# Optimization experiments

Hardware: AMD Instinct MI355X
Metric: run time of the kernel (lower is better)

Reference implementation:

```python
import jax, jax.numpy as jnp
import numpy as np
from jax import lax

B, T_IN, T_OUT = 64, 200, 400
D_ENC, D_ARNN, D_DRNN = 512, 1024, 1024
PRENET, ATT_DIM, NFILT, KSIZE, NMEL = 256, 128, 32, 31, 80


def setup_inputs() -> dict:
    key = jax.random.key(0)
    ks = jax.random.split(key, 20)
    sc = lambda k, shape: (jax.random.normal(k, shape, jnp.float32) * 0.02)
    lengths = jnp.maximum(jax.random.randint(ks[0], (B,), 0, T_IN), T_IN // 2)
    return {
        'encoder_outputs': jax.random.normal(ks[1], (B, T_IN, D_ENC), jnp.float32),
        'decoder_inputs': jax.random.normal(ks[2], (T_OUT, B, NMEL), jnp.float32),
        'encoder_outputs_lengths': lengths,
        'W_p1': sc(ks[3], (PRENET, NMEL)),
        'W_p2': sc(ks[4], (PRENET, PRENET)),
        'W_ih_a': sc(ks[5], (4 * D_ARNN, PRENET + D_ENC)),
        'W_hh_a': sc(ks[6], (4 * D_ARNN, D_ARNN)),
        'b_a': jnp.zeros((4 * D_ARNN,), jnp.float32),
        'Wq': sc(ks[7], (ATT_DIM, D_ARNN)),
        'Wmem': sc(ks[8], (ATT_DIM, D_ENC)),
        'v': sc(ks[9], (ATT_DIM,)),
        'Wconv': sc(ks[10], (NFILT, 2, KSIZE)),
        'Wloc': sc(ks[11], (ATT_DIM, NFILT)),
        'W_ih_d': sc(ks[12], (4 * D_DRNN, D_ARNN + D_ENC)),
        'W_hh_d': sc(ks[13], (4 * D_DRNN, D_DRNN)),
        'b_d': jnp.zeros((4 * D_DRNN,), jnp.float32),
        'Wp': sc(ks[14], (NMEL, D_DRNN + D_ENC)),
        'bp': jnp.zeros((NMEL,), jnp.float32),
    }


def _lstm_cell(x, h, c, Wih, Whh, b):
    g = x @ Wih.T + h @ Whh.T + b
    i, f, gg, o = jnp.split(g, 4, axis=-1)
    c_new = jax.nn.sigmoid(f) * c + jax.nn.sigmoid(i) * jnp.tanh(gg)
    h_new = jax.nn.sigmoid(o) * jnp.tanh(c_new)
    return h_new, c_new


def reference(encoder_outputs, decoder_inputs, encoder_outputs_lengths,
              W_p1, W_p2, W_ih_a, W_hh_a, b_a, Wq, Wmem, v, Wconv, Wloc,
              W_ih_d, W_hh_d, b_d, Wp, bp):
    Bsz, T_in, _ = encoder_outputs.shape
    T_steps = decoder_inputs.shape[0]
    NEG = jnp.float32(-1e8)
    pad = (KSIZE - 1) // 2

    # go frame + prenet (prenet_dropout = 0.0 => pure relu MLP)
    go = jnp.zeros((1, Bsz, NMEL), decoder_inputs.dtype)
    di = jnp.concatenate([go, decoder_inputs], axis=0)          # [T+1, B, 80]
    pre = jax.nn.relu(jax.nn.relu(di @ W_p1.T) @ W_p2.T)        # [T+1, B, 256]
    xs = pre[:T_steps]                                          # step i uses pre[i]

    processed_memory = encoder_outputs @ Wmem.T                 # [B, T_in, att]
    mask = jnp.arange(T_in)[None, :] >= encoder_outputs_lengths[:, None]

    def step(carry, x_t):
        ah, ac, dh, dc, aw, aw_cum, actx = carry
        cell_in = jnp.concatenate([x_t, actx], axis=-1)
        ah, ac = _lstm_cell(cell_in, ah, ac, W_ih_a, W_hh_a, b_a)
        # location-sensitive attention
        awc = jnp.stack([aw, aw_cum], axis=1)                   # [B, 2, T_in]
        loc = lax.conv_general_dilated(awc, Wconv, (1,), [(pad, pad)],
                                       dimension_numbers=('NCH', 'OIH', 'NCH'))
        loc = jnp.swapaxes(loc, 1, 2) @ Wloc.T                  # [B, T_in, att]
        pq = (ah @ Wq.T)[:, None, :]                            # [B, 1, att]
        energies = jnp.tanh(pq + loc + processed_memory) @ v    # [B, T_in]
        energies = jnp.where(mask, NEG, energies)
        aw = jax.nn.softmax(energies, axis=1)
        actx = jnp.einsum('bt,bte->be', aw, encoder_outputs)
        aw_cum = aw_cum + aw
        dec_in = jnp.concatenate([ah, actx], axis=-1)
        dh, dc = _lstm_cell(dec_in, dh, dc, W_ih_d, W_hh_d, b_d)
        out = jnp.concatenate([dh, actx], axis=-1) @ Wp.T + bp  # [B, 80]
        return (ah, ac, dh, dc, aw, aw_cum, actx), (out, aw)

    z = lambda d: jnp.zeros((Bsz, d), encoder_outputs.dtype)
    carry0 = (z(D_ARNN), z(D_ARNN), z(D_DRNN), z(D_DRNN), z(T_in), z(T_in), z(D_ENC))
    _, (outs, aligns) = lax.scan(step, carry0, xs)
    return jnp.swapaxes(outs, 0, 1), jnp.swapaxes(aligns, 0, 1)  # [B,T,80], [B,T,T_in]
```

## Files before the change

### kernel.cpp

```cpp
#include <hip/hip_runtime.h>
#include <cstddef>
#include <cstdint>

#define T_INN 200
#define T_OUTT 400
#define BB 64
#define DENC 512
#define NMEL 80

typedef unsigned short u16;
typedef __bf16 bf16x8 __attribute__((ext_vector_type(8)));
typedef float f32x4 __attribute__((ext_vector_type(4)));

__device__ __forceinline__ float sigf(float x) {
  return __builtin_amdgcn_rcpf(1.0f + __expf(-x));
}
__device__ __forceinline__ float ftanh(float x) {
  float e2 = __expf(2.0f * x);
  return 1.0f - 2.0f * __builtin_amdgcn_rcpf(e2 + 1.0f);
}

__device__ __forceinline__ u16 f2bf(float f) {
  unsigned u = __float_as_uint(f);
  unsigned r = u + 0x7fffu + ((u >> 16) & 1u);
  return (u16)(r >> 16);
}

__device__ __forceinline__ bf16x8 ldbf8(const u16* p) { return *(const bf16x8*)p; }

__global__ __launch_bounds__(256) void gemm_pre_kernel(
    const float* __restrict__ A, int lda, const float* __restrict__ W, int ldw,
    float* __restrict__ C, u16* __restrict__ Cbf, int ldc, int K, int relu)
{
  __shared__ float As[16][66];
  __shared__ float Ws[16][66];
  const int tid = threadIdx.x;
  const int tn = tid & 15, tm = tid >> 4;
  const int n0 = blockIdx.x * 64;
  const int m0 = blockIdx.y * 64;
  float acc[4][4] = {{0.f}};
  for (int kt = 0; kt < K; kt += 16) {
#pragma unroll
    for (int i = 0; i < 4; i++) {
      int e = tid + 256 * i;
      int m = e >> 4, kk = e & 15;
      As[kk][m] = A[(size_t)(m0 + m) * lda + kt + kk];
    }
#pragma unroll
    for (int i = 0; i < 4; i++) {
      int e = tid + 256 * i;
      int n = e >> 4, kk = e & 15;
      Ws[kk][n] = W[(size_t)(n0 + n) * ldw + kt + kk];
    }
    __syncthreads();
#pragma unroll
    for (int kk = 0; kk < 16; kk++) {
      float2 a01 = *(const float2*)&As[kk][tm * 4];
      float2 a23 = *(const float2*)&As[kk][tm * 4 + 2];
      float2 w01 = *(const float2*)&Ws[kk][tn * 4];
      float2 w23 = *(const float2*)&Ws[kk][tn * 4 + 2];
      float a[4] = {a01.x, a01.y, a23.x, a23.y};
      float w[4] = {w01.x, w01.y, w23.x, w23.y};
#pragma unroll
      for (int mi = 0; mi < 4; mi++)
#pragma unroll
        for (int ni = 0; ni < 4; ni++)
          acc[mi][ni] = fmaf(a[mi], w[ni], acc[mi][ni]);
    }
    __syncthreads();
  }
#pragma unroll
  for (int mi = 0; mi < 4; mi++) {
    int m = m0 + tm * 4 + mi;
    float v0 = acc[mi][0], v1 = acc[mi][1], v2 = acc[mi][2], v3 = acc[mi][3];
    if (relu) {
      v0 = fmaxf(v0, 0.f); v1 = fmaxf(v1, 0.f);
      v2 = fmaxf(v2, 0.f); v3 = fmaxf(v3, 0.f);
    }
    if (Cbf) {
      u16* p = Cbf + (size_t)m * ldc + n0 + tn * 4;
      p[0] = f2bf(v0); p[1] = f2bf(v1); p[2] = f2bf(v2); p[3] = f2bf(v3);
    } else {
      float4 vv; vv.x = v0; vv.y = v1; vv.z = v2; vv.w = v3;
      *(float4*)&C[(size_t)m * ldc + n0 + tn * 4] = vv;
    }
  }
}

__global__ __launch_bounds__(256) void pack_w_kernel(
    const float* __restrict__ W, u16* __restrict__ P,
    int K, int KTl, int ktOff, int KTtot, int total)
{
  int slot = blockIdx.x * 256 + threadIdx.x;
  if (slot >= total) return;
  int lane = slot & 63;
  int ktl = (slot >> 6) % KTl;
  int nt = slot / (64 * KTl);
  int n = nt * 16 + (lane & 15);
  int k = ktl * 32 + (lane >> 4) * 8;
  const float* src = W + (size_t)n * K + k;
  u16 tmp[8];
#pragma unroll
  for (int i = 0; i < 8; i++) tmp[i] = f2bf(src[i]);
  u16* dst = P + ((size_t)(nt * KTtot + (ktl + ktOff)) * 64 + lane) * 8;
  *(uint4*)dst = *(const uint4*)tmp;
}

__global__ void transpose_pm_kernel(const float* __restrict__ pm, float* __restrict__ pmT)
{
  int b = blockIdx.z;
  int tT = blockIdx.x * 32, aT = blockIdx.y * 32;
  __shared__ float tile[32][33];
  int tx = threadIdx.x, ty = threadIdx.y;
#pragma unroll
  for (int i = 0; i < 4; i++) {
    int t = tT + ty + i * 8;
    int a = aT + tx;
    if (t < T_INN) tile[ty + i * 8][tx] = pm[((size_t)b * T_INN + t) * 128 + a];
  }
  __syncthreads();
#pragma unroll
  for (int i = 0; i < 4; i++) {
    int a = aT + ty + i * 8;
    int t = tT + tx;
    if (t < T_INN) pmT[((size_t)b * 128 + a) * T_INN + t] = tile[tx][ty + i * 8];
  }
}

struct SmemGates {
  float part[16][16][66];
  float gred[1024];
};

__global__ __launch_bounds__(1024) void gates_kernel(
    const u16* __restrict__ xs,
    const u16* __restrict__ actx_bf,
    const u16* __restrict__ ah_bf_r, u16* __restrict__ ah_bf_w,
    const u16* __restrict__ dh_bf_r, u16* __restrict__ dh_bf_w,
    const u16* __restrict__ Wa, const u16* __restrict__ Wd,
    const float* __restrict__ b_a, const float* __restrict__ b_d,
    float* __restrict__ ah, float* __restrict__ ac,
    float* __restrict__ dh, float* __restrict__ dc, int t)
{
  const int z = blockIdx.z;
  if (z == 0 && t >= T_OUTT) return;
  if (z == 1 && t < 1) return;
  const int bq = blockIdx.x, ms = blockIdx.y;
  const int tid = threadIdx.x;
  const int kw = tid >> 6, lane = tid & 63;
  const int mrow = lane & 15, ksub = (lane >> 4) * 8;
  const int row = ms * 16 + mrow;
  __shared__ SmemGates sg;

  f32x4 acc0 = {0.f, 0.f, 0.f, 0.f};
  f32x4 acc1 = acc0, acc2 = acc0, acc3 = acc0;
  const float* bias; float* hF; float* cSt; u16* hw;

  if (z == 0) {
    constexpr int KT = 64;
    const size_t gstride = (size_t)KT * 32768;
    const u16* wb0 = Wa + ((size_t)(bq * KT + kw * 4) * 64 + lane) * 8;
    const u16* rb;
    if (kw < 2)      rb = xs      + (size_t)row * 256  + ksub + kw * 128;
    else if (kw < 6) rb = actx_bf + (size_t)row * 512  + ksub + kw * 128 - 256;
    else             rb = ah_bf_r + (size_t)row * 1024 + ksub + kw * 128 - 768;
#pragma unroll
    for (int i = 0; i < 4; i++) {
      bf16x8 a = ldbf8(rb + i * 32);
      const u16* wb = wb0 + (size_t)i * 512;
      bf16x8 w0 = ldbf8(wb);
      bf16x8 w1 = ldbf8(wb + gstride);
      bf16x8 w2 = ldbf8(wb + 2 * gstride);
      bf16x8 w3 = ldbf8(wb + 3 * gstride);
      acc0 = __builtin_amdgcn_mfma_f32_16x16x32_bf16(a, w0, acc0, 0, 0, 0);
      acc1 = __builtin_amdgcn_mfma_f32_16x16x32_bf16(a, w1, acc1, 0, 0, 0);
      acc2 = __builtin_amdgcn_mfma_f32_16x16x32_bf16(a, w2, acc2, 0, 0, 0);
      acc3 = __builtin_amdgcn_mfma_f32_16x16x32_bf16(a, w3, acc3, 0, 0, 0);
    }
    bias = b_a; hF = ah; cSt = ac; hw = ah_bf_w;
  } else {
    constexpr int KT = 80;
    const size_t gstride = (size_t)KT * 32768;
    const u16* wb0 = Wd + ((size_t)(bq * KT + kw) * 64 + lane) * 8;
    const u16* a0b = ah_bf_r + (size_t)row * 1024 + ksub + kw * 32;
    const u16* a1b = actx_bf + (size_t)row * 512  + ksub + kw * 32;
    const u16* a2b = dh_bf_r + (size_t)row * 1024 + ksub + kw * 32;
#pragma unroll
    for (int i = 0; i < 5; i++) {
      const u16* ap = (i < 2) ? (a0b + i * 512) : ((i == 2) ? a1b : (a2b + (i - 3) * 512));
      bf16x8 a = ldbf8(ap);
      const u16* wb = wb0 + (size_t)i * (16 * 512);
      bf16x8 w0 = ldbf8(wb);
      bf16x8 w1 = ldbf8(wb + gstride);
      bf16x8 w2 = ldbf8(wb + 2 * gstride);
      bf16x8 w3 = ldbf8(wb + 3 * gstride);
      acc0 = __builtin_amdgcn_mfma_f32_16x16x32_bf16(a, w0, acc0, 0, 0, 0);
      acc1 = __builtin_amdgcn_mfma_f32_16x16x32_bf16(a, w1, acc1, 0, 0, 0);
      acc2 = __builtin_amdgcn_mfma_f32_16x16x32_bf16(a, w2, acc2, 0, 0, 0);
      acc3 = __builtin_amdgcn_mfma_f32_16x16x32_bf16(a, w3, acc3, 0, 0, 0);
    }
    bias = b_d; hF = dh; cSt = dc; hw = dh_bf_w;
  }

#pragma unroll
  for (int r = 0; r < 4; r++) {
    sg.part[kw][r][lane]      = acc0[r];
    sg.part[kw][4 + r][lane]  = acc1[r];
    sg.part[kw][8 + r][lane]  = acc2[r];
    sg.part[kw][12 + r][lane] = acc3[r];
  }
  __syncthreads();
  {
    int g = tid >> 8, rc = tid & 255, rw = rc >> 4, col = rc & 15;
    int ln = ((rw >> 2) << 4) + col;
    int r = g * 4 + (rw & 3);
    float s = 0.f;
#pragma unroll
    for (int k2 = 0; k2 < 16; k2++) s += sg.part[k2][r][ln];
    sg.gred[tid] = s;
  }
  __syncthreads();
  if (tid < 256) {
    int rw = tid >> 4, col = tid & 15;
    int j = bq * 16 + col, m = ms * 16 + rw;
    size_t idx = (size_t)m * 1024 + j;
    float gi = sg.gred[tid]       + bias[j];
    float gf = sg.gred[256 + tid] + bias[j + 1024];
    float gg = sg.gred[512 + tid] + bias[j + 2048];
    float go = sg.gred[768 + tid] + bias[j + 3072];
    float cn = sigf(gf) * cSt[idx] + sigf(gi) * ftanh(gg);
    cSt[idx] = cn;
    float hn = sigf(go) * ftanh(cn);
    hF[idx] = hn;
    hw[idx] = f2bf(hn);
  }
}

__global__ __launch_bounds__(1024, 4) void fused_step_kernel(
    const float* __restrict__ ah, const float* __restrict__ dh,
    float* __restrict__ actx , u16* __restrict__ actx_bf,
    float* __restrict__ aw, float* __restrict__ awcum,
    const float* __restrict__ pmT, const float* __restrict__ Wq,
    const float* __restrict__ Wconv, const float* __restrict__ Wloc,
    const float* __restrict__ vvec, const int* __restrict__ lens,
    const float* __restrict__ enc, const float* __restrict__ Wp,
    const float* __restrict__ bp,
    float* __restrict__ outsOut, float* __restrict__ alignsOut, int t)
{
  const int tid = threadIdx.x;

  if (blockIdx.x >= 64) {
    if (t < 1) return;
    const int bo = blockIdx.x - 64;
    const float* actxR = actx + (size_t)((t - 1) & 1) * 32768;
    __shared__ float cp[1024];
    float s = 0.f;
    int m = tid / 12, sub = tid - m * 12;
    if (tid < 960) {
      const float4* w4 = (const float4*)(Wp + (size_t)m * 1536 + sub * 128);
      const float4* a4 = (sub < 8)
          ? (const float4*)(dh + (size_t)bo * 1024 + sub * 128)
          : (const float4*)(actxR + (size_t)bo * 512 + (sub - 8) * 128);
#pragma unroll 8
      for (int kk = 0; kk < 32; kk++) {
        float4 w = w4[kk], av = a4[kk];
        s += w.x * av.x + w.y * av.y + w.z * av.z + w.w * av.w;
      }
    }
    cp[tid] = s;
    __syncthreads();
    if (tid < 80) {
      float acc2 = bp[tid];
#pragma unroll
      for (int i2 = 0; i2 < 12; i2++) acc2 += cp[tid * 12 + i2];
      outsOut[((size_t)bo * T_OUTT + (t - 1)) * NMEL + tid] = acc2;
    }
    return;
  }

  if (t >= T_OUTT) return;
  const int b = blockIdx.x;
  const int g = tid >> 8, ti = tid & 255;
  float* actxW = actx + (size_t)(t & 1) * 32768;

  __shared__ float2 acS[T_INN];
  __shared__ float ahS[1024];
  __shared__ float pp[128][9];
  __shared__ float pqS[128];
  __shared__ float convS[T_INN][33];
  __shared__ float ep[4][256];
  __shared__ float red[256];
  __shared__ float awS[256];
  __shared__ float cpart[1024];

  if (tid < T_INN) {
    float2 v; v.x = aw[b * T_INN + tid]; v.y = awcum[b * T_INN + tid];
    acS[tid] = v;
  }
  ahS[tid] = ah[(size_t)b * 1024 + tid];
  __syncthreads();
  {
    int a = tid >> 3, kc = tid & 7;
    const float4* wv = (const float4*)(Wq + (size_t)a * 1024 + kc * 128);
    const float4* hv = (const float4*)(ahS + kc * 128);
    float s = 0.f;
#pragma unroll 8
    for (int i = 0; i < 32; i++) {
      float4 wq = wv[i], hh = hv[i];
      s += wq.x * hh.x + wq.y * hh.y + wq.z * hh.z + wq.w * hh.w;
    }
    pp[a][kc] = s;
  }
  __syncthreads();
  if (tid < 128) {
    float s = 0.f;
#pragma unroll
    for (int kc = 0; kc < 8; kc++) s += pp[tid][kc];
    pqS[tid] = s;
  }
  if (ti < T_INN) {
    float sacc[8] = {0.f, 0.f, 0.f, 0.f, 0.f, 0.f, 0.f, 0.f};
#pragma unroll
    for (int k = 0; k < 31; k++) {
      int tt = ti + k - 15;
      if (tt >= 0 && tt < T_INN) {
        float2 v = acS[tt];
#pragma unroll
        for (int f8 = 0; f8 < 8; f8++) {
          int f = g * 8 + f8;
          sacc[f8] += Wconv[f * 62 + k] * v.x + Wconv[f * 62 + 31 + k] * v.y;
        }
      }
    }
#pragma unroll
    for (int f8 = 0; f8 < 8; f8++) convS[ti][g * 8 + f8] = sacc[f8];
  }
  __syncthreads();
  float e = 0.f;
  if (ti < T_INN) {
    float cv[32];
#pragma unroll
    for (int f = 0; f < 32; f++) cv[f] = convS[ti][f];
    const float* pm = pmT + ((size_t)b * 128 + g * 32) * T_INN + ti;
#pragma unroll 4
    for (int aa = 0; aa < 32; aa++) {
      int a = g * 32 + aa;
      float x = pqS[a] + pm[(size_t)aa * T_INN];
      const float* wl = Wloc + a * 32;
#pragma unroll
      for (int f = 0; f < 32; f++) x += wl[f] * cv[f];
      float ex2 = __expf(2.f * x);
      e += vvec[a] * (1.f - 2.f * __builtin_amdgcn_rcpf(ex2 + 1.f));
    }
  }
  ep[g][ti] = e;
  __syncthreads();
  float ev = -3.0e38f, ex = 0.f;
  if (tid < 256) {
    if (tid < T_INN) {
      ev = ep[0][tid] + ep[1][tid] + ep[2][tid] + ep[3][tid];
      if (tid >= lens[b]) ev = -100000000.0f;
    }
    red[tid] = ev;
  }
  __syncthreads();
  for (int s2 = 128; s2 > 0; s2 >>= 1) {
    if (tid < s2) red[tid] = fmaxf(red[tid], red[tid + s2]);
    __syncthreads();
  }
  float mx = red[0];
  __syncthreads();
  if (tid < 256) { ex = (tid < T_INN) ? __expf(ev - mx) : 0.f; red[tid] = ex; }
  __syncthreads();
  for (int s2 = 128; s2 > 0; s2 >>= 1) {
    if (tid < s2) red[tid] += red[tid + s2];
    __syncthreads();
  }
  float inv = 1.0f / red[0];
  if (tid < T_INN) {
    float a = ex * inv;
    awS[tid] = a;
    aw[b * T_INN + tid] = a;
    awcum[b * T_INN + tid] = acS[tid].y + a;
    alignsOut[((size_t)b * T_OUTT + t) * T_INN + tid] = a;
  }
  __syncthreads();
  {
    int e0 = tid & 511, half = tid >> 9;
    const float* ep2 = enc + ((size_t)b * T_INN + half * 100) * DENC + e0;
    float s = 0.f;
#pragma unroll 4
    for (int tt = 0; tt < 100; tt++) s += awS[half * 100 + tt] * ep2[(size_t)tt * DENC];
    cpart[tid] = s;
  }
  __syncthreads();
  if (tid < 512) {
    float v2 = cpart[tid] + cpart[512 + tid];
    actxW[b * DENC + tid] = v2;
    actx_bf[b * DENC + tid] = f2bf(v2);
  }
}

extern "C" void kernel_launch(void* const* d_in, const int* in_sizes, int n_in,
                              void* d_out, int out_size, void* d_ws, size_t ws_size,
                              hipStream_t stream)
{
  const float* enc    = (const float*)d_in[0];
  const float* dec    = (const float*)d_in[1];
  const int*   lens   = (const int*)d_in[2];
  const float* W_p1   = (const float*)d_in[3];
  const float* W_p2   = (const float*)d_in[4];
  const float* W_ih_a = (const float*)d_in[5];
  const float* W_hh_a = (const float*)d_in[6];
  const float* b_a    = (const float*)d_in[7];
  const float* Wq     = (const float*)d_in[8];
  const float* Wmem   = (const float*)d_in[9];
  const float* vvec   = (const float*)d_in[10];
  const float* Wconv  = (const float*)d_in[11];
  const float* Wloc   = (const float*)d_in[12];
  const float* W_ih_d = (const float*)d_in[13];
  const float* W_hh_d = (const float*)d_in[14];
  const float* b_d    = (const float*)d_in[15];
  const float* Wp     = (const float*)d_in[16];
  const float* bp     = (const float*)d_in[17];

  float* ws = (float*)d_ws;
  size_t off = 0;
  u16* xs_bf = (u16*)(ws + off); off += (size_t)T_OUTT * 64 * 256 / 2;
  float* pmT = ws + off; off += (size_t)64 * 128 * T_INN;
  u16* Wa_pack = (u16*)(ws + off); off += (size_t)4096 * 2048 / 2;
  u16* Wd_pack = (u16*)(ws + off); off += (size_t)4096 * 2560 / 2;
  float* stateBase = ws + off;
  float* ah    = stateBase;
  float* dh    = ah + 65536;
  float* ac    = dh + 65536;
  float* dc    = ac + 65536;
  float* actx  = dc + 65536;
  float* aw    = actx + 2 * 32768;
  float* awcum = aw + 12800;
  u16* ah_bf   = (u16*)(awcum + 12800);
  u16* dh_bf   = ah_bf + 2 * 65536;
  u16* actx_bf = dh_bf + 2 * 65536;
  size_t stateFloats = 4 * 65536 + 2 * 32768 + 2 * 12800
                     + (2 * 65536 + 2 * 65536 + 32768) / 2;
  off += stateFloats;
  float* scratch = ws + off;
  float* h1 = scratch;
  float* pmt = scratch;

  float* outsOut   = (float*)d_out;
  float* alignsOut = outsOut + (size_t)BB * T_OUTT * NMEL;

  hipMemsetAsync(stateBase, 0, stateFloats * sizeof(float), stream);
  hipMemsetAsync(xs_bf, 0, (size_t)64 * 256 * sizeof(u16), stream);
  hipMemsetAsync(Wa_pack, 0, (size_t)4096 * 2048 * sizeof(u16), stream);

  {
    int tot;
    tot = 256 * 24 * 64;
    pack_w_kernel<<<(tot + 255) / 256, 256, 0, stream>>>(W_ih_a, Wa_pack, 768, 24, 0, 64, tot);
    tot = 256 * 32 * 64;
    pack_w_kernel<<<(tot + 255) / 256, 256, 0, stream>>>(W_hh_a, Wa_pack, 1024, 32, 24, 64, tot);
    tot = 256 * 48 * 64;
    pack_w_kernel<<<(tot + 255) / 256, 256, 0, stream>>>(W_ih_d, Wd_pack, 1536, 48, 0, 80, tot);
    tot = 256 * 32 * 64;
    pack_w_kernel<<<(tot + 255) / 256, 256, 0, stream>>>(W_hh_d, Wd_pack, 1024, 32, 48, 80, tot);
  }
  gemm_pre_kernel<<<dim3(4, 399), 256, 0, stream>>>(dec, 80, W_p1, 80, h1, nullptr, 256, 80, 1);
  gemm_pre_kernel<<<dim3(4, 399), 256, 0, stream>>>(h1, 256, W_p2, 256, nullptr, xs_bf + 64 * 256, 256, 256, 1);
  gemm_pre_kernel<<<dim3(2, 200), 256, 0, stream>>>(enc, 512, Wmem, 512, pmt, nullptr, 128, 512, 0);
  transpose_pm_kernel<<<dim3(7, 4, 64), dim3(32, 8), 0, stream>>>(pmt, pmT);

  for (int t = 0; t <= T_OUTT; t++) {
    int tc = (t < T_OUTT) ? t : 0;
    gates_kernel<<<dim3(64, 4, 2), 1024, 0, stream>>>(
        xs_bf + (size_t)tc * 64 * 256,
        actx_bf,
        ah_bf + (size_t)((t + 1) & 1) * 65536, ah_bf + (size_t)(t & 1) * 65536,
        dh_bf + (size_t)(t & 1) * 65536,       dh_bf + (size_t)((t + 1) & 1) * 65536,
        Wa_pack, Wd_pack, b_a, b_d, ah, ac, dh, dc, t);
    fused_step_kernel<<<128, 1024, 0, stream>>>(
        ah, dh, actx, actx_bf, aw, awcum, pmT, Wq, Wconv, Wloc, vvec,
        lens, enc, Wp, bp, outsOut, alignsOut, t);
  }
}
```

Baseline: 34.57 ms.

## Split LSTM gate GEMM into K-partial sums and move cell update into step kernel

The gates kernel now writes raw K-split partial gate sums, with two K chunks of 64 batch rows per block, to a global scratch buffer instead of reducing and applying the LSTM nonlinearity in-block. The fused step kernel sums the partials, adds the bias and performs both LSTM cell updates before the attention work. This removes the double-buffered h state and a second shared-memory reduction pass. The output projection moves into a third z-slice of the gates grid, which shifts the pipeline by one more step. It adds global traffic for the partial sums (2×64×4096 floats per LSTM per step) in exchange for more parallel blocks and fewer in-block reductions.

```diff
diff --git a/kernel.cpp b/kernel.cpp
--- a/kernel.cpp
+++ b/kernel.cpp
@@ -127,46 +127,75 @@
   }
 }
 
-struct SmemGates {
-  float part[16][16][66];
-  float gred[1024];
-};
-
 __global__ __launch_bounds__(1024) void gates_kernel(
     const u16* __restrict__ xs,
     const u16* __restrict__ actx_bf,
-    const u16* __restrict__ ah_bf_r, u16* __restrict__ ah_bf_w,
-    const u16* __restrict__ dh_bf_r, u16* __restrict__ dh_bf_w,
+    const u16* __restrict__ ah_bf,
+    const u16* __restrict__ dh_bf,
     const u16* __restrict__ Wa, const u16* __restrict__ Wd,
-    const float* __restrict__ b_a, const float* __restrict__ b_d,
-    float* __restrict__ ah, float* __restrict__ ac,
-    float* __restrict__ dh, float* __restrict__ dc, int t)
+    float* __restrict__ gpa, float* __restrict__ gpd,
+    const float* __restrict__ dh,
+    const float* __restrict__ actx,
+    const float* __restrict__ Wp, const float* __restrict__ bp,
+    float* __restrict__ outsOut, int t)
 {
-  const int z = blockIdx.z;
-  if (z == 0 && t >= T_OUTT) return;
-  if (z == 1 && t < 1) return;
-  const int bq = blockIdx.x, ms = blockIdx.y;
+  const int q = blockIdx.x, kc = blockIdx.y, z = blockIdx.z;
   const int tid = threadIdx.x;
-  const int kw = tid >> 6, lane = tid & 63;
+
+  __shared__ float part[4][4][16][66];
+
+  if (z == 2) {
+    if (t < 2) return;
+    const int bo = q;
+    const float* actxR = actx + (size_t)(t & 1) * 32768;
+    float* cp = (float*)part;
+    int mloc = tid / 12, sub = tid - mloc * 12;
+    if (tid < 480) {
+      int m = kc * 40 + mloc;
+      const float4* w4 = (const float4*)(Wp + (size_t)m * 1536 + sub * 128);
+      const float4* a4 = (sub < 8)
+          ? (const float4*)(dh + (size_t)bo * 1024 + sub * 128)
+          : (const float4*)(actxR + (size_t)bo * 512 + (sub - 8) * 128);
+      float s = 0.f;
+#pragma unroll 8
+      for (int kk = 0; kk < 32; kk++) {
+        float4 w = w4[kk], av = a4[kk];
+        s += w.x * av.x + w.y * av.y + w.z * av.z + w.w * av.w;
+      }
+      cp[tid] = s;
+    }
+    __syncthreads();
+    if (tid < 40) {
+      float acc2 = bp[kc * 40 + tid];
+#pragma unroll
+      for (int i2 = 0; i2 < 12; i2++) acc2 += cp[tid * 12 + i2];
+      outsOut[((size_t)bo * T_OUTT + (t - 2)) * NMEL + kc * 40 + tid] = acc2;
+    }
+    return;
+  }
+
+  const int wv = tid >> 6, lane = tid & 63;
+  const int kw = wv & 3, msw = wv >> 2;
   const int mrow = lane & 15, ksub = (lane >> 4) * 8;
-  const int row = ms * 16 + mrow;
-  __shared__ SmemGates sg;
+  const int row = msw * 16 + mrow;
 
   f32x4 acc0 = {0.f, 0.f, 0.f, 0.f};
   f32x4 acc1 = acc0, acc2 = acc0, acc3 = acc0;
-  const float* bias; float* hF; float* cSt; u16* hw;
+  float* gp;
 
   if (z == 0) {
-    constexpr int KT = 64;
-    const size_t gstride = (size_t)KT * 32768;
-    const u16* wb0 = Wa + ((size_t)(bq * KT + kw * 4) * 64 + lane) * 8;
-    const u16* rb;
-    if (kw < 2)      rb = xs      + (size_t)row * 256  + ksub + kw * 128;
-    else if (kw < 6) rb = actx_bf + (size_t)row * 512  + ksub + kw * 128 - 256;
-    else             rb = ah_bf_r + (size_t)row * 1024 + ksub + kw * 128 - 768;
-#pragma unroll
-    for (int i = 0; i < 4; i++) {
-      bf16x8 a = ldbf8(rb + i * 32);
+    if (t >= T_OUTT) return;
+    const size_t gstride = (size_t)64 * 32768;
+    const int kt0 = kc * 32 + kw * 8;
+    const u16* wb0 = Wa + ((size_t)(q * 64 + kt0) * 64 + lane) * 8;
+    const u16* xsb = xs      + (size_t)row * 256  + ksub;
+    const u16* axb = actx_bf + (size_t)row * 512  + ksub - 256;
+    const u16* ahb = ah_bf   + (size_t)row * 1024 + ksub - 768;
+#pragma unroll
+    for (int i = 0; i < 8; i++) {
+      int kb = (kt0 + i) * 32;
+      const u16* ap = (kb < 256) ? (xsb + kb) : ((kb < 768) ? (axb + kb) : (ahb + kb));
+      bf16x8 a = ldbf8(ap);
       const u16* wb = wb0 + (size_t)i * 512;
       bf16x8 w0 = ldbf8(wb);
       bf16x8 w1 = ldbf8(wb + gstride);
@@ -177,19 +206,21 @@
       acc2 = __builtin_amdgcn_mfma_f32_16x16x32_bf16(a, w2, acc2, 0, 0, 0);
       acc3 = __builtin_amdgcn_mfma_f32_16x16x32_bf16(a, w3, acc3, 0, 0, 0);
     }
-    bias = b_a; hF = ah; cSt = ac; hw = ah_bf_w;
+    gp = gpa;
   } else {
-    constexpr int KT = 80;
-    const size_t gstride = (size_t)KT * 32768;
-    const u16* wb0 = Wd + ((size_t)(bq * KT + kw) * 64 + lane) * 8;
-    const u16* a0b = ah_bf_r + (size_t)row * 1024 + ksub + kw * 32;
-    const u16* a1b = actx_bf + (size_t)row * 512  + ksub + kw * 32;
-    const u16* a2b = dh_bf_r + (size_t)row * 1024 + ksub + kw * 32;
-#pragma unroll
-    for (int i = 0; i < 5; i++) {
-      const u16* ap = (i < 2) ? (a0b + i * 512) : ((i == 2) ? a1b : (a2b + (i - 3) * 512));
+    if (t < 1 || t > T_OUTT) return;
+    const size_t gstride = (size_t)80 * 32768;
+    const int kt0 = kc * 40 + kw * 10;
+    const u16* wb0 = Wd + ((size_t)(q * 80 + kt0) * 64 + lane) * 8;
+    const u16* ahb = ah_bf   + (size_t)row * 1024 + ksub;
+    const u16* axb = actx_bf + (size_t)row * 512  + ksub - 1024;
+    const u16* dhb = dh_bf   + (size_t)row * 1024 + ksub - 1536;
+#pragma unroll
+    for (int i = 0; i < 10; i++) {
+      int kb = (kt0 + i) * 32;
+      const u16* ap = (kb < 1024) ? (ahb + kb) : ((kb < 1536) ? (axb + kb) : (dhb + kb));
       bf16x8 a = ldbf8(ap);
-      const u16* wb = wb0 + (size_t)i * (16 * 512);
+      const u16* wb = wb0 + (size_t)i * 512;
       bf16x8 w0 = ldbf8(wb);
       bf16x8 w1 = ldbf8(wb + gstride);
       bf16x8 w2 = ldbf8(wb + 2 * gstride);
@@ -199,89 +230,46 @@
       acc2 = __builtin_amdgcn_mfma_f32_16x16x32_bf16(a, w2, acc2, 0, 0, 0);
       acc3 = __builtin_amdgcn_mfma_f32_16x16x32_bf16(a, w3, acc3, 0, 0, 0);
     }
-    bias = b_d; hF = dh; cSt = dc; hw = dh_bf_w;
+    gp = gpd;
   }
 
 #pragma unroll
   for (int r = 0; r < 4; r++) {
-    sg.part[kw][r][lane]      = acc0[r];
-    sg.part[kw][4 + r][lane]  = acc1[r];
-    sg.part[kw][8 + r][lane]  = acc2[r];
-    sg.part[kw][12 + r][lane] = acc3[r];
+    part[msw][kw][r][lane]      = acc0[r];
+    part[msw][kw][4 + r][lane]  = acc1[r];
+    part[msw][kw][8 + r][lane]  = acc2[r];
+    part[msw][kw][12 + r][lane] = acc3[r];
   }
   __syncthreads();
   {
-    int g = tid >> 8, rc = tid & 255, rw = rc >> 4, col = rc & 15;
+    int msw2 = tid >> 8, rc = tid & 255, rw = rc >> 4, col = rc & 15;
     int ln = ((rw >> 2) << 4) + col;
-    int r = g * 4 + (rw & 3);
-    float s = 0.f;
-#pragma unroll
-    for (int k2 = 0; k2 < 16; k2++) s += sg.part[k2][r][ln];
-    sg.gred[tid] = s;
-  }
-  __syncthreads();
-  if (tid < 256) {
-    int rw = tid >> 4, col = tid & 15;
-    int j = bq * 16 + col, m = ms * 16 + rw;
-    size_t idx = (size_t)m * 1024 + j;
-    float gi = sg.gred[tid]       + bias[j];
-    float gf = sg.gred[256 + tid] + bias[j + 1024];
-    float gg = sg.gred[512 + tid] + bias[j + 2048];
-    float go = sg.gred[768 + tid] + bias[j + 3072];
-    float cn = sigf(gf) * cSt[idx] + sigf(gi) * ftanh(gg);
-    cSt[idx] = cn;
-    float hn = sigf(go) * ftanh(cn);
-    hF[idx] = hn;
-    hw[idx] = f2bf(hn);
+    float* dst = gp + ((size_t)(kc * 64 + msw2 * 16 + rw)) * 4096 + q * 16 + col;
+#pragma unroll
+    for (int g = 0; g < 4; g++) {
+      int r = g * 4 + (rw & 3);
+      float s = part[msw2][0][r][ln] + part[msw2][1][r][ln]
+              + part[msw2][2][r][ln] + part[msw2][3][r][ln];
+      dst[(size_t)g * 1024] = s;
+    }
   }
 }
 
 __global__ __launch_bounds__(1024, 4) void fused_step_kernel(
-    const float* __restrict__ ah, const float* __restrict__ dh,
+    const float* __restrict__ gpa, const float* __restrict__ gpd,
+    const float* __restrict__ b_a, const float* __restrict__ b_d,
+    float* __restrict__ ac, float* __restrict__ dc, float* __restrict__ dh,
+    u16* __restrict__ ah_bf, u16* __restrict__ dh_bf,
     float* __restrict__ actx , u16* __restrict__ actx_bf,
     float* __restrict__ aw, float* __restrict__ awcum,
     const float* __restrict__ pmT, const float* __restrict__ Wq,
     const float* __restrict__ Wconv, const float* __restrict__ Wloc,
     const float* __restrict__ vvec, const int* __restrict__ lens,
-    const float* __restrict__ enc, const float* __restrict__ Wp,
-    const float* __restrict__ bp,
-    float* __restrict__ outsOut, float* __restrict__ alignsOut, int t)
+    const float* __restrict__ enc,
+    float* __restrict__ alignsOut, int t)
 {
-  const int tid = threadIdx.x;
-
-  if (blockIdx.x >= 64) {
-    if (t < 1) return;
-    const int bo = blockIdx.x - 64;
-    const float* actxR = actx + (size_t)((t - 1) & 1) * 32768;
-    __shared__ float cp[1024];
-    float s = 0.f;
-    int m = tid / 12, sub = tid - m * 12;
-    if (tid < 960) {
-      const float4* w4 = (const float4*)(Wp + (size_t)m * 1536 + sub * 128);
-      const float4* a4 = (sub < 8)
-          ? (const float4*)(dh + (size_t)bo * 1024 + sub * 128)
-          : (const float4*)(actxR + (size_t)bo * 512 + (sub - 8) * 128);
-#pragma unroll 8
-      for (int kk = 0; kk < 32; kk++) {
-        float4 w = w4[kk], av = a4[kk];
-        s += w.x * av.x + w.y * av.y + w.z * av.z + w.w * av.w;
-      }
-    }
-    cp[tid] = s;
-    __syncthreads();
-    if (tid < 80) {
-      float acc2 = bp[tid];
-#pragma unroll
-      for (int i2 = 0; i2 < 12; i2++) acc2 += cp[tid * 12 + i2];
-      outsOut[((size_t)bo * T_OUTT + (t - 1)) * NMEL + tid] = acc2;
-    }
-    return;
-  }
-
-  if (t >= T_OUTT) return;
-  const int b = blockIdx.x;
+  const int b = blockIdx.x, tid = threadIdx.x;
   const int g = tid >> 8, ti = tid & 255;
-  float* actxW = actx + (size_t)(t & 1) * 32768;
 
   __shared__ float2 acS[T_INN];
   __shared__ float ahS[1024];
@@ -293,11 +281,41 @@
   __shared__ float awS[256];
   __shared__ float cpart[1024];
 
+  const size_t idx = (size_t)b * 1024 + tid;
+
+  if (t >= 1) {
+    const float* d0 = gpd + (size_t)b * 4096;
+    const float* d1 = gpd + (size_t)(64 + b) * 4096;
+    float gi = d0[tid]        + d1[tid]        + b_d[tid];
+    float gf = d0[tid + 1024] + d1[tid + 1024] + b_d[tid + 1024];
+    float gg = d0[tid + 2048] + d1[tid + 2048] + b_d[tid + 2048];
+    float go = d0[tid + 3072] + d1[tid + 3072] + b_d[tid + 3072];
+    float cn = sigf(gf) * dc[idx] + sigf(gi) * ftanh(gg);
+    dc[idx] = cn;
+    float hn = sigf(go) * ftanh(cn);
+    dh[idx] = hn;
+    dh_bf[idx] = f2bf(hn);
+  }
+  if (t < T_OUTT) {
+    const float* a0 = gpa + (size_t)b * 4096;
+    const float* a1 = gpa + (size_t)(64 + b) * 4096;
+    float gi = a0[tid]        + a1[tid]        + b_a[tid];
+    float gf = a0[tid + 1024] + a1[tid + 1024] + b_a[tid + 1024];
+    float gg = a0[tid + 2048] + a1[tid + 2048] + b_a[tid + 2048];
+    float go = a0[tid + 3072] + a1[tid + 3072] + b_a[tid + 3072];
+    float cn = sigf(gf) * ac[idx] + sigf(gi) * ftanh(gg);
+    ac[idx] = cn;
+    float hn = sigf(go) * ftanh(cn);
+    ah_bf[idx] = f2bf(hn);
+    ahS[tid] = hn;
+  }
+  if (t >= T_OUTT) return;
+
+  float* actxW = actx + (size_t)(t & 1) * 32768;
   if (tid < T_INN) {
     float2 v; v.x = aw[b * T_INN + tid]; v.y = awcum[b * T_INN + tid];
     acS[tid] = v;
   }
-  ahS[tid] = ah[(size_t)b * 1024 + tid];
   __syncthreads();
   {
     int a = tid >> 3, kc = tid & 7;
@@ -431,22 +449,23 @@
   u16* Wa_pack = (u16*)(ws + off); off += (size_t)4096 * 2048 / 2;
   u16* Wd_pack = (u16*)(ws + off); off += (size_t)4096 * 2560 / 2;
   float* stateBase = ws + off;
-  float* ah    = stateBase;
-  float* dh    = ah + 65536;
+  float* dh    = stateBase;
   float* ac    = dh + 65536;
   float* dc    = ac + 65536;
   float* actx  = dc + 65536;
   float* aw    = actx + 2 * 32768;
   float* awcum = aw + 12800;
   u16* ah_bf   = (u16*)(awcum + 12800);
-  u16* dh_bf   = ah_bf + 2 * 65536;
-  u16* actx_bf = dh_bf + 2 * 65536;
-  size_t stateFloats = 4 * 65536 + 2 * 32768 + 2 * 12800
-                     + (2 * 65536 + 2 * 65536 + 32768) / 2;
+  u16* dh_bf   = ah_bf + 65536;
+  u16* actx_bf = dh_bf + 65536;
+  size_t stateFloats = 3 * 65536 + 2 * 32768 + 2 * 12800
+                     + (65536 + 65536 + 32768) / 2;
   off += stateFloats;
   float* scratch = ws + off;
   float* h1 = scratch;
   float* pmt = scratch;
+  float* gpa = scratch;
+  float* gpd = scratch + (size_t)2 * 64 * 4096;
 
   float* outsOut   = (float*)d_out;
   float* alignsOut = outsOut + (size_t)BB * T_OUTT * NMEL;
@@ -471,16 +490,14 @@
   gemm_pre_kernel<<<dim3(2, 200), 256, 0, stream>>>(enc, 512, Wmem, 512, pmt, nullptr, 128, 512, 0);
   transpose_pm_kernel<<<dim3(7, 4, 64), dim3(32, 8), 0, stream>>>(pmt, pmT);
 
-  for (int t = 0; t <= T_OUTT; t++) {
+  for (int t = 0; t <= T_OUTT + 1; t++) {
     int tc = (t < T_OUTT) ? t : 0;
-    gates_kernel<<<dim3(64, 4, 2), 1024, 0, stream>>>(
-        xs_bf + (size_t)tc * 64 * 256,
-        actx_bf,
-        ah_bf + (size_t)((t + 1) & 1) * 65536, ah_bf + (size_t)(t & 1) * 65536,
-        dh_bf + (size_t)(t & 1) * 65536,       dh_bf + (size_t)((t + 1) & 1) * 65536,
-        Wa_pack, Wd_pack, b_a, b_d, ah, ac, dh, dc, t);
-    fused_step_kernel<<<128, 1024, 0, stream>>>(
-        ah, dh, actx, actx_bf, aw, awcum, pmT, Wq, Wconv, Wloc, vvec,
-        lens, enc, Wp, bp, outsOut, alignsOut, t);
-  }
-}
+    gates_kernel<<<dim3(64, 2, 3), 1024, 0, stream>>>(
+        xs_bf + (size_t)tc * 64 * 256, actx_bf, ah_bf, dh_bf,
+        Wa_pack, Wd_pack, gpa, gpd, dh, actx, Wp, bp, outsOut, t);
+    if (t <= T_OUTT)
+      fused_step_kernel<<<64, 1024, 0, stream>>>(
+          gpa, gpd, b_a, b_d, ac, dc, dh, ah_bf, dh_bf, actx, actx_bf,
+          aw, awcum, pmT, Wq, Wconv, Wloc, vvec, lens, enc, alignsOut, t);
+  }
+}
```

New measurement: 39.42 ms. 1.14x slower.

## Process two 16-row batch tiles per gates block to reuse weight loads

Applied to the files above, without the earlier changes.

Each gates block now computes 32 batch rows instead of 16, so every loaded weight fragment feeds two sets of MFMAs, and the grid's y dimension is halved. This cuts global weight traffic per step in half. The cost is twice the accumulator registers, two serialized shared-memory reduction passes with an extra barrier, and half as many blocks to spread across CUs. Launch bounds are also tightened to request four waves per SIMD.

```diff
diff --git a/kernel.cpp b/kernel.cpp
--- a/kernel.cpp
+++ b/kernel.cpp
@@ -132,7 +132,7 @@
   float gred[1024];
 };
 
-__global__ __launch_bounds__(1024) void gates_kernel(
+__global__ __launch_bounds__(1024, 4) void gates_kernel(
     const u16* __restrict__ xs,
     const u16* __restrict__ actx_bf,
     const u16* __restrict__ ah_bf_r, u16* __restrict__ ah_bf_w,
@@ -145,94 +145,128 @@
   const int z = blockIdx.z;
   if (z == 0 && t >= T_OUTT) return;
   if (z == 1 && t < 1) return;
-  const int bq = blockIdx.x, ms = blockIdx.y;
+  const int bq = blockIdx.x, ms2 = blockIdx.y;
   const int tid = threadIdx.x;
   const int kw = tid >> 6, lane = tid & 63;
   const int mrow = lane & 15, ksub = (lane >> 4) * 8;
-  const int row = ms * 16 + mrow;
+  const int rowL = ms2 * 32 + mrow;
+  const int rowH = rowL + 16;
   __shared__ SmemGates sg;
 
-  f32x4 acc0 = {0.f, 0.f, 0.f, 0.f};
-  f32x4 acc1 = acc0, acc2 = acc0, acc3 = acc0;
+  f32x4 zero4 = {0.f, 0.f, 0.f, 0.f};
+  f32x4 aL0 = zero4, aL1 = zero4, aL2 = zero4, aL3 = zero4;
+  f32x4 aH0 = zero4, aH1 = zero4, aH2 = zero4, aH3 = zero4;
   const float* bias; float* hF; float* cSt; u16* hw;
 
   if (z == 0) {
     constexpr int KT = 64;
     const size_t gstride = (size_t)KT * 32768;
     const u16* wb0 = Wa + ((size_t)(bq * KT + kw * 4) * 64 + lane) * 8;
-    const u16* rb;
-    if (kw < 2)      rb = xs      + (size_t)row * 256  + ksub + kw * 128;
-    else if (kw < 6) rb = actx_bf + (size_t)row * 512  + ksub + kw * 128 - 256;
-    else             rb = ah_bf_r + (size_t)row * 1024 + ksub + kw * 128 - 768;
+    const u16* rbL; const u16* rbH;
+    if (kw < 2) {
+      rbL = xs + (size_t)rowL * 256 + ksub + kw * 128;
+      rbH = xs + (size_t)rowH * 256 + ksub + kw * 128;
+    } else if (kw < 6) {
+      rbL = actx_bf + (size_t)rowL * 512 + ksub + kw * 128 - 256;
+      rbH = actx_bf + (size_t)rowH * 512 + ksub + kw * 128 - 256;
+    } else {
+      rbL = ah_bf_r + (size_t)rowL * 1024 + ksub + kw * 128 - 768;
+      rbH = ah_bf_r + (size_t)rowH * 1024 + ksub + kw * 128 - 768;
+    }
 #pragma unroll
     for (int i = 0; i < 4; i++) {
-      bf16x8 a = ldbf8(rb + i * 32);
+      bf16x8 al = ldbf8(rbL + i * 32);
+      bf16x8 ahi = ldbf8(rbH + i * 32);
       const u16* wb = wb0 + (size_t)i * 512;
       bf16x8 w0 = ldbf8(wb);
       bf16x8 w1 = ldbf8(wb + gstride);
       bf16x8 w2 = ldbf8(wb + 2 * gstride);
       bf16x8 w3 = ldbf8(wb + 3 * gstride);
-      acc0 = __builtin_amdgcn_mfma_f32_16x16x32_bf16(a, w0, acc0, 0, 0, 0);
-      acc1 = __builtin_amdgcn_mfma_f32_16x16x32_bf16(a, w1, acc1, 0, 0, 0);
-      acc2 = __builtin_amdgcn_mfma_f32_16x16x32_bf16(a, w2, acc2, 0, 0, 0);
-      acc3 = __builtin_amdgcn_mfma_f32_16x16x32_bf16(a, w3, acc3, 0, 0, 0);
+      aL0 = __builtin_amdgcn_mfma_f32_16x16x32_bf16(al, w0, aL0, 0, 0, 0);
+      aL1 = __builtin_amdgcn_mfma_f32_16x16x32_bf16(al, w1, aL1, 0, 0, 0);
+      aL2 = __builtin_amdgcn_mfma_f32_16x16x32_bf16(al, w2, aL2, 0, 0, 0);
+      aL3 = __builtin_amdgcn_mfma_f32_16x16x32_bf16(al, w3, aL3, 0, 0, 0);
+      aH0 = __builtin_amdgcn_mfma_f32_16x16x32_bf16(ahi, w0, aH0, 0, 0, 0);
+      aH1 = __builtin_amdgcn_mfma_f32_16x16x32_bf16(ahi, w1, aH1, 0, 0, 0);
+      aH2 = __builtin_amdgcn_mfma_f32_16x16x32_bf16(ahi, w2, aH2, 0, 0, 0);
+      aH3 = __builtin_amdgcn_mfma_f32_16x16x32_bf16(ahi, w3, aH3, 0, 0, 0);
     }
     bias = b_a; hF = ah; cSt = ac; hw = ah_bf_w;
   } else {
     constexpr int KT = 80;
     const size_t gstride = (size_t)KT * 32768;
     const u16* wb0 = Wd + ((size_t)(bq * KT + kw) * 64 + lane) * 8;
-    const u16* a0b = ah_bf_r + (size_t)row * 1024 + ksub + kw * 32;
-    const u16* a1b = actx_bf + (size_t)row * 512  + ksub + kw * 32;
-    const u16* a2b = dh_bf_r + (size_t)row * 1024 + ksub + kw * 32;
+    const u16* a0L = ah_bf_r + (size_t)rowL * 1024 + ksub + kw * 32;
+    const u16* a1L = actx_bf + (size_t)rowL * 512  + ksub + kw * 32;
+    const u16* a2L = dh_bf_r + (size_t)rowL * 1024 + ksub + kw * 32;
+    const u16* a0H = ah_bf_r + (size_t)rowH * 1024 + ksub + kw * 32;
+    const u16* a1H = actx_bf + (size_t)rowH * 512  + ksub + kw * 32;
+    const u16* a2H = dh_bf_r + (size_t)rowH * 1024 + ksub + kw * 32;
 #pragma unroll
     for (int i = 0; i < 5; i++) {
-      const u16* ap = (i < 2) ? (a0b + i * 512) : ((i == 2) ? a1b : (a2b + (i - 3) * 512));
-      bf16x8 a = ldbf8(ap);
+      const u16* apL = (i < 2) ? (a0L + i * 512) : ((i == 2) ? a1L : (a2L + (i - 3) * 512));
+      const u16* apH = (i < 2) ? (a0H + i * 512) : ((i == 2) ? a1H : (a2H + (i - 3) * 512));
+      bf16x8 al = ldbf8(apL);
+      bf16x8 ahi = ldbf8(apH);
       const u16* wb = wb0 + (size_t)i * (16 * 512);
       bf16x8 w0 = ldbf8(wb);
       bf16x8 w1 = ldbf8(wb + gstride);
       bf16x8 w2 = ldbf8(wb + 2 * gstride);
       bf16x8 w3 = ldbf8(wb + 3 * gstride);
-      acc0 = __builtin_amdgcn_mfma_f32_16x16x32_bf16(a, w0, acc0, 0, 0, 0);
-      acc1 = __builtin_amdgcn_mfma_f32_16x16x32_bf16(a, w1, acc1, 0, 0, 0);
-      acc2 = __builtin_amdgcn_mfma_f32_16x16x32_bf16(a, w2, acc2, 0, 0, 0);
-      acc3 = __builtin_amdgcn_mfma_f32_16x16x32_bf16(a, w3, acc3, 0, 0, 0);
+      aL0 = __builtin_amdgcn_mfma_f32_16x16x32_bf16(al, w0, aL0, 0, 0, 0);
+      aL1 = __builtin_amdgcn_mfma_f32_16x16x32_bf16(al, w1, aL1, 0, 0, 0);
+      aL2 = __builtin_amdgcn_mfma_f32_16x16x32_bf16(al, w2, aL2, 0, 0, 0);
+      aL3 = __builtin_amdgcn_mfma_f32_16x16x32_bf16(al, w3, aL3, 0, 0, 0);
+      aH0 = __builtin_amdgcn_mfma_f32_16x16x32_bf16(ahi, w0, aH0, 0, 0, 0);
+      aH1 = __builtin_amdgcn_mfma_f32_16x16x32_bf16(ahi, w1, aH1, 0, 0, 0);
+      aH2 = __builtin_amdgcn_mfma_f32_16x16x32_bf16(ahi, w2, aH2, 0, 0, 0);
+      aH3 = __builtin_amdgcn_mfma_f32_16x16x32_bf16(ahi, w3, aH3, 0, 0, 0);
     }
     bias = b_d; hF = dh; cSt = dc; hw = dh_bf_w;
   }
 
 #pragma unroll
-  for (int r = 0; r < 4; r++) {
-    sg.part[kw][r][lane]      = acc0[r];
-    sg.part[kw][4 + r][lane]  = acc1[r];
-    sg.part[kw][8 + r][lane]  = acc2[r];
-    sg.part[kw][12 + r][lane] = acc3[r];
-  }
-  __syncthreads();
-  {
-    int g = tid >> 8, rc = tid & 255, rw = rc >> 4, col = rc & 15;
-    int ln = ((rw >> 2) << 4) + col;
-    int r = g * 4 + (rw & 3);
-    float s = 0.f;
-#pragma unroll
-    for (int k2 = 0; k2 < 16; k2++) s += sg.part[k2][r][ln];
-    sg.gred[tid] = s;
-  }
-  __syncthreads();
-  if (tid < 256) {
-    int rw = tid >> 4, col = tid & 15;
-    int j = bq * 16 + col, m = ms * 16 + rw;
-    size_t idx = (size_t)m * 1024 + j;
-    float gi = sg.gred[tid]       + bias[j];
-    float gf = sg.gred[256 + tid] + bias[j + 1024];
-    float gg = sg.gred[512 + tid] + bias[j + 2048];
-    float go = sg.gred[768 + tid] + bias[j + 3072];
-    float cn = sigf(gf) * cSt[idx] + sigf(gi) * ftanh(gg);
-    cSt[idx] = cn;
-    float hn = sigf(go) * ftanh(cn);
-    hF[idx] = hn;
-    hw[idx] = f2bf(hn);
+  for (int h = 0; h < 2; h++) {
+    if (h == 1) __syncthreads();
+#pragma unroll
+    for (int r = 0; r < 4; r++) {
+      if (h == 0) {
+        sg.part[kw][r][lane]      = aL0[r];
+        sg.part[kw][4 + r][lane]  = aL1[r];
+        sg.part[kw][8 + r][lane]  = aL2[r];
+        sg.part[kw][12 + r][lane] = aL3[r];
+      } else {
+        sg.part[kw][r][lane]      = aH0[r];
+        sg.part[kw][4 + r][lane]  = aH1[r];
+        sg.part[kw][8 + r][lane]  = aH2[r];
+        sg.part[kw][12 + r][lane] = aH3[r];
+      }
+    }
+    __syncthreads();
+    {
+      int g = tid >> 8, rc = tid & 255, rw = rc >> 4, col = rc & 15;
+      int ln = ((rw >> 2) << 4) + col;
+      int r = g * 4 + (rw & 3);
+      float s = 0.f;
+#pragma unroll
+      for (int k2 = 0; k2 < 16; k2++) s += sg.part[k2][r][ln];
+      sg.gred[tid] = s;
+    }
+    __syncthreads();
+    if (tid < 256) {
+      int rw = tid >> 4, col = tid & 15;
+      int j = bq * 16 + col, m = ms2 * 32 + h * 16 + rw;
+      size_t idx = (size_t)m * 1024 + j;
+      float gi = sg.gred[tid]       + bias[j];
+      float gf = sg.gred[256 + tid] + bias[j + 1024];
+      float gg = sg.gred[512 + tid] + bias[j + 2048];
+      float go = sg.gred[768 + tid] + bias[j + 3072];
+      float cn = sigf(gf) * cSt[idx] + sigf(gi) * ftanh(gg);
+      cSt[idx] = cn;
+      float hn = sigf(go) * ftanh(cn);
+      hF[idx] = hn;
+      hw[idx] = f2bf(hn);
+    }
   }
 }
 
@@ -473,7 +507,7 @@
 
   for (int t = 0; t <= T_OUTT; t++) {
     int tc = (t < T_OUTT) ? t : 0;
-    gates_kernel<<<dim3(64, 4, 2), 1024, 0, stream>>>(
+    gates_kernel<<<dim3(64, 2, 2), 1024, 0, stream>>>(
         xs_bf + (size_t)tc * 64 * 256,
         actx_bf,
         ah_bf + (size_t)((t + 1) & 1) * 65536, ah_bf + (size_t)(t & 1) * 65536,
```

New measurement: 33.82 ms. 2.2% less time.
